# Kernel tuning notes

Measured on AMD Instinct MI355X. Metric: run time of the kernel, lower is better.

The kernel has to match this reference:

```python
import math
import jax, jax.numpy as jnp
import numpy as np

B, SX, SY, D, H = 2, 1024, 1024, 1024, 16
FULL = 1536   # padded (full_q == full_k) frame length for the two-source attention
N_CTX = 2048  # causal bias buffer size
HD = D // H
LENS_X = np.array([1024, 700])
LENS_Y = np.array([1024, 850])


def _heads(t):
    b, s, d = t.shape
    return t.reshape(b, s, H, HD).transpose(0, 2, 1, 3)  # [B,H,S,HD]


def _merge(t):
    b, h, s, hd = t.shape
    return t.transpose(0, 2, 1, 3).reshape(b, s, h * hd)


def setup_inputs() -> dict:
    key = jax.random.key(0)
    ks = jax.random.split(key, 8)
    s = 0.02
    # ragged pack/unpack index lists: take = positions in the FULL frame, fill = positions in the shrunk frame
    x_take_b = np.concatenate([np.full(l, b, np.int32) for b, l in enumerate(LENS_X)])
    x_take_p = np.concatenate([(FULL - l + np.arange(l)).astype(np.int32) for l in LENS_X])  # right-aligned
    x_fill_b = x_take_b.copy()
    x_fill_p = np.concatenate([np.arange(l, dtype=np.int32) for l in LENS_X])
    y_take_b = np.concatenate([np.full(l, b, np.int32) for b, l in enumerate(LENS_Y)])
    y_take_p = np.concatenate([np.arange(l, dtype=np.int32) for l in LENS_Y])  # left-aligned
    y_fill_b = y_take_b.copy()
    y_fill_p = y_take_p.copy()
    # additive padding mask for the self-attention over shrunk x
    mask = np.full((B, 1, 1, SX), -10000.0, np.float32)
    for b, l in enumerate(LENS_X):
        mask[b, :, :, :l] = 0.0
    return {
        "x": jax.random.normal(ks[0], (B, SX, D), jnp.float32),
        "y": jax.random.normal(ks[1], (B, SY, D), jnp.float32),
        "attention_mask_x": jnp.asarray(mask),
        "W_attn": jax.random.normal(ks[2], (D, 3 * D), jnp.float32) * s,
        "b_attn": jnp.zeros((3 * D,), jnp.float32),
        "W_2a": jax.random.normal(ks[3], (D, D), jnp.float32) * s,
        "b_2a": jnp.zeros((D,), jnp.float32),
        "W_2b": jax.random.normal(ks[4], (D, 2 * D), jnp.float32) * s,
        "b_2b": jnp.zeros((2 * D,), jnp.float32),
        "W_proj": jax.random.normal(ks[5], (2 * D, D), jnp.float32) * s,
        "b_proj": jnp.zeros((D,), jnp.float32),
        "x_take_b": jnp.asarray(x_take_b), "x_take_p": jnp.asarray(x_take_p),
        "x_fill_b": jnp.asarray(x_fill_b), "x_fill_p": jnp.asarray(x_fill_p),
        "y_take_b": jnp.asarray(y_take_b), "y_take_p": jnp.asarray(y_take_p),
        "y_fill_b": jnp.asarray(y_fill_b), "y_fill_p": jnp.asarray(y_fill_p),
    }


def reference(x, y, attention_mask_x, W_attn, b_attn, W_2a, b_2a, W_2b, b_2b,
              W_proj, b_proj, x_take_b, x_take_p, x_fill_b, x_fill_p,
              y_take_b, y_take_p, y_fill_b, y_fill_p):
    causal = jnp.tril(jnp.ones((N_CTX, N_CTX), jnp.float32))
    inv_sqrt = 1.0 / math.sqrt(HD)

    # --- branch 1: causal self-attention on shrunk x ---
    qkv = x @ W_attn + b_attn
    q, k, v = jnp.split(qkv, 3, axis=2)
    q, k, v = _heads(q), _heads(k), _heads(v)
    w = jnp.einsum('bhqd,bhkd->bhqk', q, k) * inv_sqrt  # [B,H,SX,SX]
    b1 = causal[:SX, :SX]
    w = w * b1 - 10000.0 * (1.0 - b1) + attention_mask_x
    a = jnp.einsum('bhqk,bhkd->bhqd', jax.nn.softmax(w, axis=-1), v)
    a = _merge(a)  # [B,SX,D]

    # --- branch 2: two-source attention with ragged expand/shrink ---
    q2 = _heads(x @ W_2a + b_2a)                      # [B,H,SX,HD]
    k2, v2 = jnp.split(y @ W_2b + b_2b, 2, axis=2)
    k2, v2 = _heads(k2), _heads(v2)                   # [B,H,SY,HD]
    w2 = jnp.einsum('bhqd,bhkd->bhqk', q2, k2)        # [B,H,SX,SY] (unscaled yet)
    # expand key dim: shrunk SY -> FULL
    temp = jnp.zeros((B, H, SX, FULL), w2.dtype)
    temp = temp.at[y_take_b, :, :, y_take_p].set(w2[y_fill_b, :, :, y_fill_p])
    # expand query dim: shrunk SX -> FULL
    new_w = jnp.zeros((B, H, FULL, FULL), w2.dtype)
    new_w = new_w.at[x_take_b, :, x_take_p, :].set(temp[x_fill_b, :, x_fill_p, :])
    new_v = jnp.zeros((B, H, FULL, HD), v2.dtype)
    new_v = new_v.at[y_take_b, :, y_take_p, :].set(v2[y_fill_b, :, y_fill_p, :])
    kmask = jnp.full((B, 1, 1, FULL), -10000.0, w2.dtype)
    kmask = kmask.at[y_take_b, :, :, y_take_p].set(0.0)
    new_w = new_w * inv_sqrt
    b2 = causal[:FULL, :FULL]  # ns-nd == 0 since full_q == full_k
    new_w = new_w * b2 - 10000.0 * (1.0 - b2) + kmask
    a2 = jnp.einsum('bhqk,bhkd->bhqd', jax.nn.softmax(new_w, axis=-1), new_v)  # [B,H,FULL,HD]
    # shrink query dim back: FULL -> SX
    a2s = jnp.zeros((B, H, SX, HD), a2.dtype)
    a2s = a2s.at[x_fill_b, :, x_fill_p, :].set(a2[x_take_b, :, x_take_p, :])
    a2m = _merge(a2s)  # [B,SX,D]

    out = jnp.concatenate([a, a2m], axis=2) @ W_proj + b_proj  # [B,SX,D]
    return out
```

## Files before the change

### kernel.cpp

```cpp
#include <hip/hip_runtime.h>
#include <hip/hip_bf16.h>

typedef __bf16 bf16;
typedef __attribute__((ext_vector_type(4))) __bf16 bf16x4;
typedef __attribute__((ext_vector_type(8))) __bf16 bf16x8;
typedef __attribute__((ext_vector_type(4))) float floatx4;

__device__ __forceinline__ void gl_lds16(const bf16* g, bf16* l) {
  __builtin_amdgcn_global_load_lds(
      (const __attribute__((address_space(1))) void*)g,
      (__attribute__((address_space(3))) void*)l, 16, 0, 0);
}

__global__ __launch_bounds__(256) void sentinel_kernel(float* out, int n, float code) {
  int i = blockIdx.x * 256 + threadIdx.x;
  if (i < n) out[i] = code;
}

struct TP { const float* W; bf16* WT; int K; int N; int bxn; int bid0; };

__global__ __launch_bounds__(256) void prep_kernel(TP t0, TP t1, TP t2, TP t3,
                                                   const float* __restrict__ x,
                                                   const float* __restrict__ y,
                                                   bf16* __restrict__ xb,
                                                   bf16* __restrict__ yb) {
  int bid = blockIdx.x;
  int tid = threadIdx.x;
  if (bid < 2048) {
    __shared__ float tile[64][65];
    TP t = t0;
    if (bid >= t3.bid0) t = t3;
    else if (bid >= t2.bid0) t = t2;
    else if (bid >= t1.bid0) t = t1;
    int rb = bid - t.bid0;
    int n0 = (rb % t.bxn) * 64, k0 = (rb / t.bxn) * 64;
    int tx = tid & 15, ty = tid >> 4;
#pragma unroll
    for (int i = 0; i < 4; ++i) {
      floatx4 v = *(const floatx4*)(t.W + (size_t)(k0 + ty + 16 * i) * t.N + n0 + tx * 4);
#pragma unroll
      for (int j = 0; j < 4; ++j) tile[ty + 16 * i][tx * 4 + j] = v[j];
    }
    __syncthreads();
#pragma unroll
    for (int i = 0; i < 4; ++i) {
      int nr = ty + 16 * i;
      bf16x4 o;
#pragma unroll
      for (int j = 0; j < 4; ++j) o[j] = (bf16)tile[tx * 4 + j][nr];
      *(bf16x4*)(t.WT + (size_t)(n0 + nr) * t.K + k0 + tx * 4) = o;
    }
  } else {
    long base = (long)(bid - 2048) * 4096 + (long)tid * 16;
    const float* src = x; bf16* dst = xb; long idx = base;
    if (base >= 2097152) { src = y; dst = yb; idx = base - 2097152; }
    floatx4 v0 = *(const floatx4*)(src + idx);
    floatx4 v1 = *(const floatx4*)(src + idx + 4);
    floatx4 v2 = *(const floatx4*)(src + idx + 8);
    floatx4 v3 = *(const floatx4*)(src + idx + 12);
    bf16x8 o0, o1;
#pragma unroll
    for (int i = 0; i < 4; ++i) {
      o0[i] = (bf16)v0[i]; o0[4 + i] = (bf16)v1[i];
      o1[i] = (bf16)v2[i]; o1[4 + i] = (bf16)v3[i];
    }
    *(bf16x8*)(dst + idx) = o0;
    *(bf16x8*)(dst + idx + 8) = o1;
  }
}

struct GP { const bf16* A; const bf16* WT; const float* bias; bf16* C; bf16* VT;
            int N; int ldc; int vcol0; int bxn; int bid0; };

__global__ __launch_bounds__(512, 2) void proj3_kernel(GP g0, GP g1, GP g2) {
  __shared__ __attribute__((aligned(16))) bf16 As[2][16384];
  __shared__ __attribute__((aligned(16))) bf16 Bs[2][16384];
  int bid = blockIdx.x;
  GP g = g0;
  if (bid >= g2.bid0) g = g2;
  else if (bid >= g1.bid0) g = g1;
  int rb = bid - g.bid0;
  int row0 = (rb / g.bxn) * 256, col0 = (rb % g.bxn) * 256;
  int tid = threadIdx.x;
  int lane = tid & 63, wave = tid >> 6;
  int quad = lane >> 4, l16 = lane & 15;
  int wm = wave >> 2, wn = wave & 3;
  const bf16* Ag = g.A + (size_t)row0 * 1024;
  const bf16* Bg = g.WT + (size_t)col0 * 1024;

  auto stA = [&](bf16* L, int k0, int qr) {
#pragma unroll
    for (int t = 0; t < 2; ++t) {
      int i = t * 512 + tid;
      int rh = i >> 3, o = i & 7;
      int m = qr * 64 + (rh & 63) + ((rh & 64) << 1);
      gl_lds16(Ag + (size_t)m * 1024 + k0 + ((o ^ (m & 7)) * 8),
               L + (size_t)(m * 8 + o) * 8);
    }
  };
  auto stB = [&](bf16* L, int k0, int qc) {
#pragma unroll
    for (int t = 0; t < 2; ++t) {
      int i = t * 512 + tid;
      int rh = i >> 3, o = i & 7;
      int n = qc * 32 + (rh & 31) + ((rh >> 5) << 6);
      gl_lds16(Bg + (size_t)n * 1024 + k0 + ((o ^ (n & 7)) * 8),
               L + (size_t)(n * 8 + o) * 8);
    }
  };

  floatx4 acc[8][4] = {};

  stA(As[0], 0, 0); stB(Bs[0], 0, 0);
  stA(As[0], 0, 1); stB(Bs[0], 0, 1);
  stB(Bs[1], 64, 0);
  stA(As[1], 64, 1);
  asm volatile("s_waitcnt vmcnt(4)" ::: "memory");
  __builtin_amdgcn_s_barrier();

#pragma unroll 2
  for (int T = 0; T < 16; ++T) {
    int cb = T & 1, nb = cb ^ 1;
    const bf16* Ac = As[cb];
    const bf16* Bc = Bs[cb];
    bf16x8 fA[2][4], fB[2][2], fA2[2][4], fB2[2][2];

#pragma unroll
    for (int kk = 0; kk < 2; ++kk) {
      int ko = kk * 4 + quad;
#pragma unroll
      for (int r = 0; r < 4; ++r) {
        int m = wm * 128 + r * 16 + l16;
        fA[kk][r] = *(const bf16x8*)(Ac + (size_t)(m * 8 + (ko ^ (m & 7))) * 8);
      }
#pragma unroll
      for (int c = 0; c < 2; ++c) {
        int n = wn * 64 + c * 16 + l16;
        fB[kk][c] = *(const bf16x8*)(Bc + (size_t)(n * 8 + (ko ^ (n & 7))) * 8);
      }
    }
    stA(As[nb], (T + 1) * 64, 0);
    asm volatile("s_waitcnt lgkmcnt(0)" ::: "memory");
    __builtin_amdgcn_s_barrier();
    __builtin_amdgcn_sched_barrier(0);
    __builtin_amdgcn_s_setprio(1);
#pragma unroll
    for (int kk = 0; kk < 2; ++kk)
#pragma unroll
      for (int r = 0; r < 4; ++r)
#pragma unroll
        for (int c = 0; c < 2; ++c)
          acc[r][c] = __builtin_amdgcn_mfma_f32_16x16x32_bf16(fA[kk][r], fB[kk][c], acc[r][c], 0, 0, 0);
    __builtin_amdgcn_s_setprio(0);
    __builtin_amdgcn_s_barrier();

#pragma unroll
    for (int kk = 0; kk < 2; ++kk) {
      int ko = kk * 4 + quad;
#pragma unroll
      for (int r = 0; r < 4; ++r) {
        int m = wm * 128 + 64 + r * 16 + l16;
        fA2[kk][r] = *(const bf16x8*)(Ac + (size_t)(m * 8 + (ko ^ (m & 7))) * 8);
      }
    }
    stB(Bs[nb], (T + 1) * 64, 1);
    asm volatile("s_waitcnt lgkmcnt(0)" ::: "memory");
    __builtin_amdgcn_s_barrier();
    __builtin_amdgcn_sched_barrier(0);
    __builtin_amdgcn_s_setprio(1);
#pragma unroll
    for (int kk = 0; kk < 2; ++kk)
#pragma unroll
      for (int r = 0; r < 4; ++r)
#pragma unroll
        for (int c = 0; c < 2; ++c)
          acc[4 + r][c] = __builtin_amdgcn_mfma_f32_16x16x32_bf16(fA2[kk][r], fB[kk][c], acc[4 + r][c], 0, 0, 0);
    __builtin_amdgcn_s_setprio(0);
    __builtin_amdgcn_s_barrier();

#pragma unroll
    for (int kk = 0; kk < 2; ++kk) {
      int ko = kk * 4 + quad;
#pragma unroll
      for (int c = 0; c < 2; ++c) {
        int n = wn * 64 + 32 + c * 16 + l16;
        fB2[kk][c] = *(const bf16x8*)(Bc + (size_t)(n * 8 + (ko ^ (n & 7))) * 8);
      }
    }
    stB(Bs[cb], (T + 2) * 64, 0);
    asm volatile("s_waitcnt lgkmcnt(0)" ::: "memory");
    __builtin_amdgcn_s_barrier();
    __builtin_amdgcn_sched_barrier(0);
    __builtin_amdgcn_s_setprio(1);
#pragma unroll
    for (int kk = 0; kk < 2; ++kk)
#pragma unroll
      for (int r = 0; r < 4; ++r)
#pragma unroll
        for (int c = 0; c < 2; ++c)
          acc[4 + r][2 + c] = __builtin_amdgcn_mfma_f32_16x16x32_bf16(fA2[kk][r], fB2[kk][c], acc[4 + r][2 + c], 0, 0, 0);
    __builtin_amdgcn_s_setprio(0);
    __builtin_amdgcn_s_barrier();

#pragma unroll
    for (int kk = 0; kk < 2; ++kk) {
      int ko = kk * 4 + quad;
#pragma unroll
      for (int r = 0; r < 4; ++r) {
        int m = wm * 128 + r * 16 + l16;
        fA[kk][r] = *(const bf16x8*)(Ac + (size_t)(m * 8 + (ko ^ (m & 7))) * 8);
      }
    }
    stA(As[cb], (T + 2) * 64, 1);
    asm volatile("s_waitcnt vmcnt(4) lgkmcnt(0)" ::: "memory");
    __builtin_amdgcn_s_barrier();
    __builtin_amdgcn_sched_barrier(0);
    __builtin_amdgcn_s_setprio(1);
#pragma unroll
    for (int kk = 0; kk < 2; ++kk)
#pragma unroll
      for (int r = 0; r < 4; ++r)
#pragma unroll
        for (int c = 0; c < 2; ++c)
          acc[r][2 + c] = __builtin_amdgcn_mfma_f32_16x16x32_bf16(fA[kk][r], fB2[kk][c], acc[r][2 + c], 0, 0, 0);
    __builtin_amdgcn_s_setprio(0);
    __builtin_amdgcn_s_barrier();
  }

  int inV = (col0 >= g.vcol0);
#pragma unroll
  for (int c = 0; c < 4; ++c) {
    int gcol = col0 + wn * 64 + c * 16 + l16;
    float bv = g.bias[gcol];
    if (inV) {
      int vcol = gcol - g.vcol0;
      int hh = vcol >> 6, dd = vcol & 63;
#pragma unroll
      for (int r = 0; r < 8; ++r) {
        int row = row0 + wm * 128 + r * 16 + quad * 4;
        int bb = row >> 10, key = row & 1023;
        bf16x4 pk;
#pragma unroll
        for (int e = 0; e < 4; ++e) pk[e] = (bf16)(acc[r][c][e] + bv);
        *(bf16x4*)(g.VT + ((size_t)((bb << 4) + hh)) * 65536 + (size_t)dd * 1024 + key) = pk;
      }
    } else {
#pragma unroll
      for (int r = 0; r < 8; ++r) {
        int grow = row0 + wm * 128 + r * 16 + quad * 4;
#pragma unroll
        for (int e = 0; e < 4; ++e)
          g.C[(size_t)(grow + e) * g.ldc + gcol] = (bf16)(acc[r][c][e] + bv);
      }
    }
  }
}

__global__ __launch_bounds__(256) void gemm_out_kernel(const bf16* __restrict__ A,
                                                       const bf16* __restrict__ WT,
                                                       const float* __restrict__ bias,
                                                       float* __restrict__ C,
                                                       int N, int K) {
  __shared__ __attribute__((aligned(16))) bf16 As[64 * 64];
  __shared__ __attribute__((aligned(16))) bf16 Bs[64 * 64];
  int tid = threadIdx.x;
  int lane = tid & 63, wave = tid >> 6;
  int quad = lane >> 4, l16 = lane & 15;
  int row0 = blockIdx.y * 64, col0 = blockIdx.x * 64;
  floatx4 acc[4] = {};
  for (int k0 = 0; k0 < K; k0 += 64) {
#pragma unroll
    for (int s = 0; s < 2; ++s) {
      int sl = s * 256 + tid;
      int r = sl >> 3, o = sl & 7;
      int c = (o ^ (r & 7)) * 8;
      gl_lds16(A + (size_t)(row0 + r) * K + k0 + c, As + (size_t)sl * 8);
      gl_lds16(WT + (size_t)(col0 + r) * K + k0 + c, Bs + (size_t)sl * 8);
    }
    __syncthreads();
#pragma unroll
    for (int kk = 0; kk < 2; ++kk) {
      int ko = kk * 4 + quad;
      int m = wave * 16 + l16;
      bf16x8 af = *(const bf16x8*)(As + (size_t)(m * 8 + (ko ^ (m & 7))) * 8);
#pragma unroll
      for (int nt = 0; nt < 4; ++nt) {
        int n = nt * 16 + l16;
        bf16x8 bf = *(const bf16x8*)(Bs + (size_t)(n * 8 + (ko ^ (n & 7))) * 8);
        acc[nt] = __builtin_amdgcn_mfma_f32_16x16x32_bf16(af, bf, acc[nt], 0, 0, 0);
      }
    }
    __syncthreads();
  }
#pragma unroll
  for (int nt = 0; nt < 4; ++nt) {
    int gcol = col0 + nt * 16 + l16;
    float bv = bias[gcol];
#pragma unroll
    for (int e = 0; e < 4; ++e) {
      int grow = row0 + wave * 16 + quad * 4 + e;
      C[(size_t)grow * N + gcol] = acc[nt][e] + bv;
    }
  }
}

struct AP {
  const bf16* Q; const bf16* K; const bf16* VT; bf16* O;
  int qstride, kstride, ostride;
  long qbatch, kbatch, obatch;
  int coff0, coff1, klen0, klen1, qv0, qv1;
};

__global__ __launch_bounds__(512) void attn2x_kernel(AP a0, AP a1, float scale) {
  __shared__ __attribute__((aligned(16))) bf16 Ks[2][64 * 64];
  __shared__ __attribute__((aligned(16))) bf16 Vs[2][64 * 64];
  __shared__ __attribute__((aligned(16))) bf16 Ps[8][16 * 72];
  AP a = (blockIdx.x >> 8) ? a1 : a0;
  int tid = threadIdx.x;
  int lane = tid & 63, w = tid >> 6;
  int quad = lane >> 4, l16 = lane & 15;
  int r = blockIdx.x & 255;
  int b = r >> 7, h = (r >> 3) & 15, qt = r & 7;
  int coff = b ? a.coff1 : a.coff0;
  int klen = b ? a.klen1 : a.klen0;
  int qv = b ? a.qv1 : a.qv0;
  int qbase = qt * 128;
  int wq0 = qbase + w * 16;
  int qi = wq0 + l16;
  const bf16* Q   = a.Q + (size_t)b * a.qbatch + h * 64;
  const bf16* Kp  = a.K + (size_t)b * a.kbatch + h * 64;
  const bf16* VTp = a.VT + (size_t)(b * 16 + h) * 65536;
  bf16* O = a.O + (size_t)b * a.obatch + h * 64;

  bf16x8 aq0 = *(const bf16x8*)(Q + (size_t)qi * a.qstride + quad * 8);
  bf16x8 aq1 = *(const bf16x8*)(Q + (size_t)qi * a.qstride + 32 + quad * 8);

  floatx4 o[4] = {};
  float part = 0.f;

  int kend = klen < qbase + 128 + coff ? klen : qbase + 128 + coff;
  int nblk = (kend + 63) >> 6;
  int wkend0 = wq0 + 16 + coff;
  int wkend = klen < wkend0 ? klen : wkend0;

  const float KSC = scale * 1.44269504f;
  const float KOFF = -5.77078016f;

  auto stage = [&](int buf, int j0) {
    int row = tid >> 3, ch = tid & 7;
    gl_lds16(Kp + (size_t)(j0 + row) * a.kstride + ((ch ^ (row & 7)) * 8),
             Ks[buf] + (size_t)tid * 8);
    gl_lds16(VTp + (size_t)row * 1024 + j0 + ((ch ^ (row & 7)) * 8),
             Vs[buf] + (size_t)tid * 8);
  };

  stage(0, 0);
  for (int t = 0; t < nblk; ++t) {
    int j0 = t * 64;
    __syncthreads();
    if (t + 1 < nblk) stage((t + 1) & 1, j0 + 64);
    if (j0 >= wkend) continue;
    const bf16* Kt = Ks[t & 1];
    const bf16* Vt = Vs[t & 1];

    floatx4 sv[4];
#pragma unroll
    for (int nt = 0; nt < 4; ++nt) {
      int key = nt * 16 + l16;
      int sl0 = key * 8 + (quad ^ (key & 7));
      int sl1 = key * 8 + ((quad + 4) ^ (key & 7));
      bf16x8 bk0 = *(const bf16x8*)(Kt + (size_t)sl0 * 8);
      bf16x8 bk1 = *(const bf16x8*)(Kt + (size_t)sl1 * 8);
      floatx4 z = {};
      z = __builtin_amdgcn_mfma_f32_16x16x32_bf16(bk0, aq0, z, 0, 0, 0);
      z = __builtin_amdgcn_mfma_f32_16x16x32_bf16(bk1, aq1, z, 0, 0, 0);
      sv[nt] = z;
    }
    bool fullv = (j0 + 63 <= wq0 + coff) && (j0 + 63 < klen);
#pragma unroll
    for (int nt = 0; nt < 4; ++nt) {
      bf16x4 pk;
#pragma unroll
      for (int e = 0; e < 4; ++e) {
        float arg = fmaf(sv[nt][e], KSC, KOFF);
        if (!fullv) {
          int j = j0 + nt * 16 + quad * 4 + e;
          arg = (j <= qi + coff && j < klen) ? arg : -60.0f;
        }
        float p = exp2f(arg);
        part += p;
        pk[e] = (bf16)p;
      }
      *(bf16x4*)(Ps[w] + l16 * 72 + nt * 16 + quad * 4) = pk;
    }
    bf16x8 pb0 = *(const bf16x8*)(Ps[w] + l16 * 72 + quad * 8);
    bf16x8 pb1 = *(const bf16x8*)(Ps[w] + l16 * 72 + 32 + quad * 8);
#pragma unroll
    for (int ct = 0; ct < 4; ++ct) {
      int dd = ct * 16 + l16;
      int sl0 = dd * 8 + (quad ^ (dd & 7));
      int sl1 = dd * 8 + ((quad + 4) ^ (dd & 7));
      bf16x8 va0 = *(const bf16x8*)(Vt + (size_t)sl0 * 8);
      bf16x8 va1 = *(const bf16x8*)(Vt + (size_t)sl1 * 8);
      o[ct] = __builtin_amdgcn_mfma_f32_16x16x32_bf16(va0, pb0, o[ct], 0, 0, 0);
      o[ct] = __builtin_amdgcn_mfma_f32_16x16x32_bf16(va1, pb1, o[ct], 0, 0, 0);
    }
  }
  part += __shfl_xor(part, 16);
  part += __shfl_xor(part, 32);
  float rinv = 1.0f / part;
#pragma unroll
  for (int ct = 0; ct < 4; ++ct) {
    bf16x4 pk;
#pragma unroll
    for (int e = 0; e < 4; ++e) {
      float val = o[ct][e] * rinv;
      if (qi >= qv) val = 0.f;
      pk[e] = (bf16)val;
    }
    *(bf16x4*)(O + (size_t)qi * a.ostride + ct * 16 + quad * 4) = pk;
  }
}

extern "C" void kernel_launch(void* const* d_in, const int* in_sizes, int n_in,
                              void* d_out, int out_size, void* d_ws, size_t ws_size,
                              hipStream_t stream) {
  const float* x      = (const float*)d_in[0];
  const float* y      = (const float*)d_in[1];
  const float* W_attn = (const float*)d_in[3];
  const float* b_attn = (const float*)d_in[4];
  const float* W_2a   = (const float*)d_in[5];
  const float* b_2a   = (const float*)d_in[6];
  const float* W_2b   = (const float*)d_in[7];
  const float* b_2b   = (const float*)d_in[8];
  const float* W_proj = (const float*)d_in[9];
  const float* b_proj = (const float*)d_in[10];
  bf16* ws = (bf16*)d_ws;
  float* out = (float*)d_out;

  const int LX0 = 1024, LX1 = 700, LY0 = 1024, LY1 = 850;
  const float scale = 0.125f;
  const size_t WS_FAST = (size_t)25165824 * 2;

  if (ws_size < WS_FAST) {
    sentinel_kernel<<<(out_size + 255) / 256, 256, 0, stream>>>(
        out, out_size, (float)(ws_size >> 20) + 10.0f);
    return;
  }

  bf16* qk1  = ws;
  bf16* q2   = ws + (size_t) 4194304;
  bf16* k2   = ws + (size_t) 6291456;
  bf16* VT1  = ws + (size_t) 8388608;
  bf16* VT2  = ws + (size_t)10485760;
  bf16* xb   = ws + (size_t)12582912;
  bf16* yb   = ws + (size_t)14680064;
  bf16* cat  = ws + (size_t)12582912;
  bf16* WaT  = ws + (size_t)16777216;
  bf16* W2aT = ws + (size_t)19922944;
  bf16* W2bT = ws + (size_t)20971520;
  bf16* WpT  = ws + (size_t)23068672;

  TP t0 = {W_attn, WaT, 1024, 3072, 48, 0};
  TP t1 = {W_2a, W2aT, 1024, 1024, 16, 768};
  TP t2 = {W_2b, W2bT, 1024, 2048, 32, 1024};
  TP t3 = {W_proj, WpT, 2048, 1024, 16, 1536};
  prep_kernel<<<3072, 256, 0, stream>>>(t0, t1, t2, t3, x, y, xb, yb);

  GP g0 = {xb, WaT, b_attn, qk1, VT1, 3072, 2048, 2048, 12, 0};
  GP g1 = {xb, W2aT, b_2a, q2, nullptr, 1024, 1024, 1 << 30, 4, 96};
  GP g2 = {yb, W2bT, b_2b, k2, VT2, 2048, 1024, 1024, 8, 128};
  proj3_kernel<<<192, 512, 0, stream>>>(g0, g1, g2);

  AP a0 = {qk1, qk1 + 1024, VT1, cat, 2048, 2048, 2048,
           (long)1024 * 2048, (long)1024 * 2048, (long)1024 * 2048,
           0, 0, LX0, LX1, 1024, 1024};
  AP a1 = {q2, k2, VT2, cat + 1024, 1024, 1024, 2048,
           (long)1024 * 1024, (long)1024 * 1024, (long)1024 * 2048,
           1536 - LX0, 1536 - LX1, LY0, LY1, LX0, LX1};
  attn2x_kernel<<<512, 512, 0, stream>>>(a0, a1, scale);

  gemm_out_kernel<<<dim3(16, 32), 256, 0, stream>>>(cat, WpT, b_proj, out, 1024, 2048);
}
```

Before: 234.2 us.

## Restructure GEMM pipeline to one barrier per quadrant and remap block order

Rewrites the main loop of the fused projection GEMM so each quadrant issues the next tile's global-to-LDS loads for the alternate buffer and uses a single barrier with partial vmcnt waits. Previously each quadrant used two barriers and the prefetch straddled buffers. The prologue now loads only the first k-tile. Block indices are also remapped with an (rawb&7)*24 + rawb>>3 swizzle, meant to spread work across XCDs for better L2 locality. The swizzle assumes exactly 192 blocks, and the reworked waitcnt and barrier accounting risks races or stalls if the counts are wrong.

```diff
diff --git a/kernel.cpp b/kernel.cpp
--- a/kernel.cpp
+++ b/kernel.cpp
@@ -75,7 +75,8 @@
 __global__ __launch_bounds__(512, 2) void proj3_kernel(GP g0, GP g1, GP g2) {
   __shared__ __attribute__((aligned(16))) bf16 As[2][16384];
   __shared__ __attribute__((aligned(16))) bf16 Bs[2][16384];
-  int bid = blockIdx.x;
+  int rawb = blockIdx.x;
+  int bid = (rawb & 7) * 24 + (rawb >> 3);
   GP g = g0;
   if (bid >= g2.bid0) g = g2;
   else if (bid >= g1.bid0) g = g1;
@@ -111,10 +112,7 @@
 
   floatx4 acc[8][4] = {};
 
-  stA(As[0], 0, 0); stB(Bs[0], 0, 0);
-  stA(As[0], 0, 1); stB(Bs[0], 0, 1);
-  stB(Bs[1], 64, 0);
-  stA(As[1], 64, 1);
+  stA(As[0], 0, 0); stB(Bs[0], 0, 0); stB(Bs[0], 0, 1); stA(As[0], 0, 1);
   asm volatile("s_waitcnt vmcnt(4)" ::: "memory");
   __builtin_amdgcn_s_barrier();
 
@@ -123,7 +121,8 @@
     int cb = T & 1, nb = cb ^ 1;
     const bf16* Ac = As[cb];
     const bf16* Bc = Bs[cb];
-    bf16x8 fA[2][4], fB[2][2], fA2[2][4], fB2[2][2];
+    int k1 = (T + 1) * 64;
+    bf16x8 fA[2][4], fB0[2][2], fB1[2][2], fA2[2][4], fB0r[2][2];
 
 #pragma unroll
     for (int kk = 0; kk < 2; ++kk) {
@@ -136,12 +135,14 @@
 #pragma unroll
       for (int c = 0; c < 2; ++c) {
         int n = wn * 64 + c * 16 + l16;
-        fB[kk][c] = *(const bf16x8*)(Bc + (size_t)(n * 8 + (ko ^ (n & 7))) * 8);
-      }
-    }
-    stA(As[nb], (T + 1) * 64, 0);
+        fB0[kk][c] = *(const bf16x8*)(Bc + (size_t)(n * 8 + (ko ^ (n & 7))) * 8);
+      }
+    }
+    stA(As[nb], k1, 0);
+    asm volatile("s_waitcnt vmcnt(4)" ::: "memory");
+    asm volatile("s_waitcnt lgkmcnt(8)" ::: "memory");
+    __builtin_amdgcn_s_barrier();
     asm volatile("s_waitcnt lgkmcnt(0)" ::: "memory");
-    __builtin_amdgcn_s_barrier();
     __builtin_amdgcn_sched_barrier(0);
     __builtin_amdgcn_s_setprio(1);
 #pragma unroll
@@ -150,9 +151,32 @@
       for (int r = 0; r < 4; ++r)
 #pragma unroll
         for (int c = 0; c < 2; ++c)
-          acc[r][c] = __builtin_amdgcn_mfma_f32_16x16x32_bf16(fA[kk][r], fB[kk][c], acc[r][c], 0, 0, 0);
+          acc[r][c] = __builtin_amdgcn_mfma_f32_16x16x32_bf16(fA[kk][r], fB0[kk][c], acc[r][c], 0, 0, 0);
     __builtin_amdgcn_s_setprio(0);
+
+#pragma unroll
+    for (int kk = 0; kk < 2; ++kk) {
+      int ko = kk * 4 + quad;
+#pragma unroll
+      for (int c = 0; c < 2; ++c) {
+        int n = wn * 64 + 32 + c * 16 + l16;
+        fB1[kk][c] = *(const bf16x8*)(Bc + (size_t)(n * 8 + (ko ^ (n & 7))) * 8);
+      }
+    }
+    stB(Bs[nb], k1, 0);
+    asm volatile("s_waitcnt vmcnt(4)" ::: "memory");
     __builtin_amdgcn_s_barrier();
+    asm volatile("s_waitcnt lgkmcnt(0)" ::: "memory");
+    __builtin_amdgcn_sched_barrier(0);
+    __builtin_amdgcn_s_setprio(1);
+#pragma unroll
+    for (int kk = 0; kk < 2; ++kk)
+#pragma unroll
+      for (int r = 0; r < 4; ++r)
+#pragma unroll
+        for (int c = 0; c < 2; ++c)
+          acc[r][2 + c] = __builtin_amdgcn_mfma_f32_16x16x32_bf16(fA[kk][r], fB1[kk][c], acc[r][2 + c], 0, 0, 0);
+    __builtin_amdgcn_s_setprio(0);
 
 #pragma unroll
     for (int kk = 0; kk < 2; ++kk) {
@@ -163,9 +187,10 @@
         fA2[kk][r] = *(const bf16x8*)(Ac + (size_t)(m * 8 + (ko ^ (m & 7))) * 8);
       }
     }
-    stB(Bs[nb], (T + 1) * 64, 1);
+    stB(Bs[nb], k1, 1);
+    asm volatile("s_waitcnt vmcnt(4)" ::: "memory");
+    __builtin_amdgcn_s_barrier();
     asm volatile("s_waitcnt lgkmcnt(0)" ::: "memory");
-    __builtin_amdgcn_s_barrier();
     __builtin_amdgcn_sched_barrier(0);
     __builtin_amdgcn_s_setprio(1);
 #pragma unroll
@@ -174,22 +199,22 @@
       for (int r = 0; r < 4; ++r)
 #pragma unroll
         for (int c = 0; c < 2; ++c)
-          acc[4 + r][c] = __builtin_amdgcn_mfma_f32_16x16x32_bf16(fA2[kk][r], fB[kk][c], acc[4 + r][c], 0, 0, 0);
+          acc[4 + r][2 + c] = __builtin_amdgcn_mfma_f32_16x16x32_bf16(fA2[kk][r], fB1[kk][c], acc[4 + r][2 + c], 0, 0, 0);
     __builtin_amdgcn_s_setprio(0);
-    __builtin_amdgcn_s_barrier();
 
 #pragma unroll
     for (int kk = 0; kk < 2; ++kk) {
       int ko = kk * 4 + quad;
 #pragma unroll
       for (int c = 0; c < 2; ++c) {
-        int n = wn * 64 + 32 + c * 16 + l16;
-        fB2[kk][c] = *(const bf16x8*)(Bc + (size_t)(n * 8 + (ko ^ (n & 7))) * 8);
-      }
-    }
-    stB(Bs[cb], (T + 2) * 64, 0);
+        int n = wn * 64 + c * 16 + l16;
+        fB0r[kk][c] = *(const bf16x8*)(Bc + (size_t)(n * 8 + (ko ^ (n & 7))) * 8);
+      }
+    }
+    stA(As[nb], k1, 1);
+    asm volatile("s_waitcnt vmcnt(4)" ::: "memory");
+    __builtin_amdgcn_s_barrier();
     asm volatile("s_waitcnt lgkmcnt(0)" ::: "memory");
-    __builtin_amdgcn_s_barrier();
     __builtin_amdgcn_sched_barrier(0);
     __builtin_amdgcn_s_setprio(1);
 #pragma unroll
@@ -198,33 +223,8 @@
       for (int r = 0; r < 4; ++r)
 #pragma unroll
         for (int c = 0; c < 2; ++c)
-          acc[4 + r][2 + c] = __builtin_amdgcn_mfma_f32_16x16x32_bf16(fA2[kk][r], fB2[kk][c], acc[4 + r][2 + c], 0, 0, 0);
+          acc[4 + r][c] = __builtin_amdgcn_mfma_f32_16x16x32_bf16(fA2[kk][r], fB0r[kk][c], acc[4 + r][c], 0, 0, 0);
     __builtin_amdgcn_s_setprio(0);
-    __builtin_amdgcn_s_barrier();
-
-#pragma unroll
-    for (int kk = 0; kk < 2; ++kk) {
-      int ko = kk * 4 + quad;
-#pragma unroll
-      for (int r = 0; r < 4; ++r) {
-        int m = wm * 128 + r * 16 + l16;
-        fA[kk][r] = *(const bf16x8*)(Ac + (size_t)(m * 8 + (ko ^ (m & 7))) * 8);
-      }
-    }
-    stA(As[cb], (T + 2) * 64, 1);
-    asm volatile("s_waitcnt vmcnt(4) lgkmcnt(0)" ::: "memory");
-    __builtin_amdgcn_s_barrier();
-    __builtin_amdgcn_sched_barrier(0);
-    __builtin_amdgcn_s_setprio(1);
-#pragma unroll
-    for (int kk = 0; kk < 2; ++kk)
-#pragma unroll
-      for (int r = 0; r < 4; ++r)
-#pragma unroll
-        for (int c = 0; c < 2; ++c)
-          acc[r][2 + c] = __builtin_amdgcn_mfma_f32_16x16x32_bf16(fA[kk][r], fB2[kk][c], acc[r][2 + c], 0, 0, 0);
-    __builtin_amdgcn_s_setprio(0);
-    __builtin_amdgcn_s_barrier();
   }
 
   int inV = (col0 >= g.vcol0);
```

Measured after the change: 226.4 us. 3.3% less time.
